# Performance work log

Hardware: AMD Instinct MI355X
Metric: run time of the kernel (lower is better)

Reference implementation:

```python
import jax, jax.numpy as jnp
import numpy as np

B, T, C, H = 4, 4096, 1024, 64

def setup_inputs() -> dict:
    key = jax.random.key(0)
    kx, kk, kq, kv = jax.random.split(key, 4)
    x = jax.random.normal(kx, (B, T, C), dtype=jnp.float32)
    # causal lower-triangular mask; masked_fill where mask == 0
    mask = jnp.tril(jnp.ones((T, T), dtype=jnp.int32))
    s = 1.0 / np.sqrt(C)
    Wk = jax.random.normal(kk, (H, C), dtype=jnp.float32) * s
    Wq = jax.random.normal(kq, (H, C), dtype=jnp.float32) * s
    Wv = jax.random.normal(kv, (H, C), dtype=jnp.float32) * s
    return {"x": x, "mask": mask, "Wk": Wk, "Wq": Wq, "Wv": Wv}

def reference(x, mask, Wk, Wq, Wv):
    # single-head attention; dropout is identity in eval mode
    scale = Wk.shape[0] ** -0.5  # head_size ** -0.5
    k = jnp.einsum('btc,hc->bth', x, Wk)  # [B,T,H]
    q = jnp.einsum('btc,hc->bth', x, Wq)
    v = jnp.einsum('btc,hc->bth', x, Wv)
    att = jnp.einsum('bqh,bkh->bqk', q, k) * scale  # [B,T,T]
    att = jnp.where(mask == 0, -jnp.inf, att)
    att = jax.nn.softmax(att, axis=-1)
    out = jnp.einsum('bqk,bkh->bqh', att, v)  # [B,T,H]
    return out
```

## Files before the change

kernel.cpp:

```cpp
#include <hip/hip_runtime.h>
#include <hip/hip_bf16.h>

#define BT 16384
#define CDIM 1024
#define HD 64
#define TT 4096

typedef __bf16 bf16x8 __attribute__((ext_vector_type(8)));
typedef __bf16 bf16x4 __attribute__((ext_vector_type(4)));
typedef float f32x4 __attribute__((ext_vector_type(4)));

__device__ __forceinline__ f32x4 mfma16(bf16x8 a, bf16x8 b, f32x4 c){
  return __builtin_amdgcn_mfma_f32_16x16x32_bf16(a, b, c, 0, 0, 0);
}

__global__ __launch_bounds__(256) void wconv_k(const float* __restrict__ Wk,
    const float* __restrict__ Wq, const float* __restrict__ Wv,
    __bf16* __restrict__ Wbf){
  int idx = blockIdx.x*256 + threadIdx.x;
  int e0 = idx*4;
  int n = e0 >> 10;
  int c = e0 & 1023;
  const float* src; float s;
  if (n < 64)      { src = Wk + (size_t)n*CDIM;       s = 1.0f;   }
  else if (n < 128){ src = Wq + (size_t)(n-64)*CDIM;  s = 0.125f; }
  else             { src = Wv + (size_t)(n-128)*CDIM; s = 1.0f;   }
  float4 v = *reinterpret_cast<const float4*>(src + c);
  __bf16* dst = Wbf + e0;
  dst[0]=(__bf16)(v.x*s); dst[1]=(__bf16)(v.y*s);
  dst[2]=(__bf16)(v.z*s); dst[3]=(__bf16)(v.w*s);
}

__global__ __launch_bounds__(256) void proj_k(const float* __restrict__ x,
    const __bf16* __restrict__ Wbf, __bf16* __restrict__ kb,
    __bf16* __restrict__ qb, __bf16* __restrict__ vTb){
  __shared__ __bf16 Wt[192][68];
  __shared__ __bf16 Xt[16][68];

  const int tid  = threadIdx.x;
  const int lane = tid & 63;
  const int w    = tid >> 6;
  const int l15  = lane & 15, g = lane >> 4;
  const long row0 = (long)blockIdx.x*16;

  int wrw[6], wc8[6];
  #pragma unroll
  for (int i=0;i<6;i++){
    const int c = tid + 256*i;
    wrw[i] = c >> 3;
    wc8[i] = (c & 7)*8;
  }
  const int xrw = tid >> 4, xc4 = (tid & 15)*4;
  const float* xsrc = x + (row0 + xrw)*CDIM + xc4;

  f32x4 acc[3];
  #pragma unroll
  for (int j=0;j<3;j++) acc[j] = (f32x4)(0.0f);

  bf16x8 wreg[6];
  float4 xr;

  #pragma unroll
  for (int i=0;i<6;i++)
    wreg[i] = *reinterpret_cast<const bf16x8*>(Wbf + (size_t)wrw[i]*CDIM + wc8[i]);
  xr = *reinterpret_cast<const float4*>(xsrc);

  for (int t=0; t<16; ++t){
    #pragma unroll
    for (int i=0;i<6;i++)
      *reinterpret_cast<bf16x8*>(&Wt[wrw[i]][wc8[i]]) = wreg[i];
    {
      bf16x4 xv;
      xv[0]=(__bf16)xr.x; xv[1]=(__bf16)xr.y; xv[2]=(__bf16)xr.z; xv[3]=(__bf16)xr.w;
      *reinterpret_cast<bf16x4*>(&Xt[xrw][xc4]) = xv;
    }
    __syncthreads();

    if (t+1 < 16){
      const int nk = (t+1)*64;
      #pragma unroll
      for (int i=0;i<6;i++)
        wreg[i] = *reinterpret_cast<const bf16x8*>(Wbf + (size_t)wrw[i]*CDIM + nk + wc8[i]);
      xr = *reinterpret_cast<const float4*>(xsrc + nk);
    }

    {
      bf16x8 a0 = *reinterpret_cast<const bf16x8*>(&Xt[l15][g*8]);
      bf16x8 a1 = *reinterpret_cast<const bf16x8*>(&Xt[l15][g*8 + 32]);
      #pragma unroll
      for (int nf=0;nf<3;nf++){
        bf16x8 b0 = *reinterpret_cast<const bf16x8*>(&Wt[w*48 + nf*16 + l15][g*8]);
        bf16x8 b1 = *reinterpret_cast<const bf16x8*>(&Wt[w*48 + nf*16 + l15][g*8 + 32]);
        acc[nf] = mfma16(a1, b1, mfma16(a0, b0, acc[nf]));
      }
    }
    __syncthreads();
  }

  const long bidx = row0 >> 12;
  #pragma unroll
  for (int nf=0;nf<3;nf++){
    const int n0  = w*48 + nf*16 + l15;
    const int mat = n0 >> 6;
    const int h   = n0 & 63;
    const long rbase = row0 + g*4;
    if (mat == 0){
      #pragma unroll
      for (int r=0;r<4;r++) kb[(rbase+r)*HD + h] = (__bf16)acc[nf][r];
    } else if (mat == 1){
      #pragma unroll
      for (int r=0;r<4;r++) qb[(rbase+r)*HD + h] = (__bf16)acc[nf][r];
    } else {
      bf16x4 t4;
      #pragma unroll
      for (int r=0;r<4;r++) t4[r] = (__bf16)acc[nf][r];
      *reinterpret_cast<bf16x4*>(vTb + (bidx*64 + h)*TT + (rbase & 4095)) = t4;
    }
  }
}

template<int NS>
__global__ __launch_bounds__(256) void attn_part_k(const __bf16* __restrict__ kbg,
    const __bf16* __restrict__ qbg, const __bf16* __restrict__ vT,
    __bf16* __restrict__ po, float* __restrict__ pl){
  __shared__ __bf16 Klds[64][68];
  __shared__ __bf16 Vlds[64][68];
  __shared__ __bf16 Plds[4][16][68];

  const int tid  = threadIdx.x;
  const int lane = tid & 63;
  const int w    = tid >> 6;
  const int l15  = lane & 15, g = lane >> 4;

  const int bi  = blockIdx.x;
  const int b   = bi / (64*NS);
  const int rem = bi % (64*NS);
  const int qt  = 63 - rem / NS;
  const int s   = rem % NS;

  const int ntiles = qt + 1;
  const int lo = ( s      * ntiles) / NS;
  const int hi = ((s + 1) * ntiles) / NS;
  const int pidx = (b*64 + qt)*NS + s;

  if (lo == hi){
    if (l15 == 0){
      #pragma unroll
      for (int r=0;r<4;r++) pl[pidx*64 + w*16 + g*4 + r] = 0.0f;
    }
    return;
  }

  const long qbase = (long)b*TT + (long)qt*64;

  bf16x8 qf0, qf1;
  {
    const __bf16* src = qbg + (qbase + w*16 + l15)*HD + g*8;
    qf0 = *reinterpret_cast<const bf16x8*>(src);
    qf1 = *reinterpret_cast<const bf16x8*>(src + 32);
  }

  f32x4 o[4];
  #pragma unroll
  for (int ch=0; ch<4; ++ch) o[ch] = (f32x4)(0.0f);
  float lp[4] = {0.f, 0.f, 0.f, 0.f};

  const __bf16* vbase = vT + (size_t)b*64*TT;

  const int skey = tid >> 2;
  const int sd0  = (tid & 3) * 16;
  bf16x8 kr0, kr1, vr0, vr1;

  {
    const long kvbase = (long)b*TT + (long)lo*64;
    const __bf16* ks = kbg + (kvbase + skey)*HD + sd0;
    kr0 = *reinterpret_cast<const bf16x8*>(ks);
    kr1 = *reinterpret_cast<const bf16x8*>(ks+8);
    const __bf16* vs = vbase + (size_t)skey*TT + lo*64 + sd0;
    vr0 = *reinterpret_cast<const bf16x8*>(vs);
    vr1 = *reinterpret_cast<const bf16x8*>(vs+8);
  }

  for (int kv=lo; kv<hi; ++kv){
    __syncthreads();
    *reinterpret_cast<bf16x8*>(&Klds[skey][sd0])   = kr0;
    *reinterpret_cast<bf16x8*>(&Klds[skey][sd0+8]) = kr1;
    *reinterpret_cast<bf16x8*>(&Vlds[skey][sd0])   = vr0;
    *reinterpret_cast<bf16x8*>(&Vlds[skey][sd0+8]) = vr1;
    __syncthreads();

    if (kv+1 < hi){
      const long nbase = (long)b*TT + (long)(kv+1)*64;
      const __bf16* ks = kbg + (nbase + skey)*HD + sd0;
      kr0 = *reinterpret_cast<const bf16x8*>(ks);
      kr1 = *reinterpret_cast<const bf16x8*>(ks+8);
      const __bf16* vs = vbase + (size_t)skey*TT + (kv+1)*64 + sd0;
      vr0 = *reinterpret_cast<const bf16x8*>(vs);
      vr1 = *reinterpret_cast<const bf16x8*>(vs+8);
    }

    f32x4 sv[4];
    __builtin_amdgcn_s_setprio(1);
    #pragma unroll
    for (int c=0;c<4;c++){
      bf16x8 kb0 = *reinterpret_cast<const bf16x8*>(&Klds[c*16 + l15][g*8]);
      bf16x8 kb1 = *reinterpret_cast<const bf16x8*>(&Klds[c*16 + l15][g*8 + 32]);
      sv[c] = mfma16(qf0, kb0, (f32x4)(-16.0f));
      sv[c] = mfma16(qf1, kb1, sv[c]);
    }
    __builtin_amdgcn_s_setprio(0);

    if (kv == qt){
      #pragma unroll
      for (int c=0;c<4;c++){
        const int key = c*16 + l15;
        #pragma unroll
        for (int r=0;r<4;r++){
          const int qr = w*16 + g*4 + r;
          if (key > qr) sv[c][r] = -1e30f;
        }
      }
    }

    #pragma unroll
    for (int c=0;c<4;c++){
      #pragma unroll
      for (int r=0;r<4;r++) sv[c][r] = __expf(sv[c][r]);
    }
    #pragma unroll
    for (int r=0;r<4;r++)
      lp[r] += (sv[0][r] + sv[1][r]) + (sv[2][r] + sv[3][r]);

    #pragma unroll
    for (int c=0;c<4;c++){
      #pragma unroll
      for (int r=0;r<4;r++) Plds[w][g*4+r][c*16 + l15] = (__bf16)sv[c][r];
    }
    asm volatile("s_waitcnt lgkmcnt(0)" ::: "memory");
    __builtin_amdgcn_sched_barrier(0);
    bf16x8 pa0 = *reinterpret_cast<const bf16x8*>(&Plds[w][l15][g*8]);
    bf16x8 pa1 = *reinterpret_cast<const bf16x8*>(&Plds[w][l15][g*8 + 32]);

    __builtin_amdgcn_s_setprio(1);
    #pragma unroll
    for (int ch=0; ch<4; ++ch){
      bf16x8 vb0 = *reinterpret_cast<const bf16x8*>(&Vlds[ch*16 + l15][g*8]);
      bf16x8 vb1 = *reinterpret_cast<const bf16x8*>(&Vlds[ch*16 + l15][g*8 + 32]);
      o[ch] = mfma16(pa0, vb0, o[ch]);
      o[ch] = mfma16(pa1, vb1, o[ch]);
    }
    __builtin_amdgcn_s_setprio(0);
  }

  float lr[4];
  #pragma unroll
  for (int r=0;r<4;r++){
    float v = lp[r];
    v += __shfl_xor(v, 1);
    v += __shfl_xor(v, 2);
    v += __shfl_xor(v, 4);
    v += __shfl_xor(v, 8);
    lr[r] = v;
  }
  float rl[4];
  #pragma unroll
  for (int r=0;r<4;r++) rl[r] = (lr[r] > 0.0f) ? 1.0f/lr[r] : 0.0f;

  __bf16* podst = po + (size_t)pidx*4096;
  #pragma unroll
  for (int ch=0; ch<4; ++ch){
    #pragma unroll
    for (int r=0;r<4;r++)
      podst[(w*16 + g*4 + r)*64 + ch*16 + l15] = (__bf16)(o[ch][r] * rl[r]);
  }
  if (l15 == 0){
    #pragma unroll
    for (int r=0;r<4;r++) pl[pidx*64 + w*16 + g*4 + r] = lr[r];
  }
}

template<int NS>
__global__ __launch_bounds__(256) void comb_k(const __bf16* __restrict__ po,
    const float* __restrict__ pl, float* __restrict__ out){
  const int idx4  = (blockIdx.x*256 + threadIdx.x)*4;
  const int qrow  = idx4 >> 6;
  const int dim0  = idx4 & 63;
  const int qtg   = qrow >> 6;
  const int rowin = qrow & 63;

  float num0=0.f, num1=0.f, num2=0.f, num3=0.f, den=0.f;
  #pragma unroll
  for (int s=0;s<NS;s++){
    const float lv = pl[(qtg*NS + s)*64 + rowin];
    den += lv;
    bf16x4 p4 = *reinterpret_cast<const bf16x4*>(
        po + (size_t)(qtg*NS + s)*4096 + rowin*64 + dim0);
    num0 += lv*(float)p4[0]; num1 += lv*(float)p4[1];
    num2 += lv*(float)p4[2]; num3 += lv*(float)p4[3];
  }
  const float rd = 1.0f/den;
  float4 o = make_float4(num0*rd, num1*rd, num2*rd, num3*rd);
  *reinterpret_cast<float4*>(out + idx4) = o;
}

extern "C" void kernel_launch(void* const* d_in, const int* in_sizes, int n_in,
                              void* d_out, int out_size, void* d_ws, size_t ws_size,
                              hipStream_t stream) {
  const float* x  = (const float*)d_in[0];
  const float* Wk = (const float*)d_in[2];
  const float* Wq = (const float*)d_in[3];
  const float* Wv = (const float*)d_in[4];
  float* out = (float*)d_out;

  char* ws = (char*)d_ws;
  __bf16* Wbf = (__bf16*)ws;
  __bf16* kb  = (__bf16*)(ws + 393216);
  __bf16* qb  = (__bf16*)(ws + 2490368);
  __bf16* vTb = (__bf16*)(ws + 4587520);
  __bf16* po  = (__bf16*)(ws + 6684672);

  wconv_k<<<192,  256, 0, stream>>>(Wk, Wq, Wv, Wbf);
  proj_k <<<1024, 256, 0, stream>>>(x, Wbf, kb, qb, vTb);

  const size_t need8 = 6684672ull + (size_t)2048*4096*2 + (size_t)2048*64*4;
  if (ws_size >= need8){
    float* pl = (float*)(ws + 6684672 + (size_t)2048*4096*2);
    attn_part_k<8><<<2048, 256, 0, stream>>>(kb, qb, vTb, po, pl);
    comb_k<8>    <<<1024, 256, 0, stream>>>(po, pl, out);
  } else {
    float* pl = (float*)(ws + 6684672 + (size_t)1024*4096*2);
    attn_part_k<4><<<1024, 256, 0, stream>>>(kb, qb, vTb, po, pl);
    comb_k<4>    <<<1024, 256, 0, stream>>>(po, pl, out);
  }
}
```

Measured before the change: 66.92 us.

## Enlarge projection tile to 32 rows and 128-wide K steps with 8 waves

The QKV projection kernel now processes 32 rows per block with 512 threads, split into two row-groups of four waves, and steps K by 128 instead of 64. Each staged weight tile is therefore reused across twice as many rows, which halves total weight traffic from global memory and halves the number of barrier iterations. The cost is larger LDS use per block (about 60 KB), possibly lower occupancy, and half as many blocks in the grid.

```diff
diff --git a/kernel.cpp b/kernel.cpp
--- a/kernel.cpp
+++ b/kernel.cpp
@@ -31,79 +31,97 @@
   dst[2]=(__bf16)(v.z*s); dst[3]=(__bf16)(v.w*s);
 }
 
-__global__ __launch_bounds__(256) void proj_k(const float* __restrict__ x,
+__global__ __launch_bounds__(512) void proj_k(const float* __restrict__ x,
     const __bf16* __restrict__ Wbf, __bf16* __restrict__ kb,
     __bf16* __restrict__ qb, __bf16* __restrict__ vTb){
-  __shared__ __bf16 Wt[192][68];
-  __shared__ __bf16 Xt[16][68];
+  __shared__ __bf16 Wt[192][136];
+  __shared__ __bf16 Xt[32][136];
 
   const int tid  = threadIdx.x;
   const int lane = tid & 63;
   const int w    = tid >> 6;
+  const int wr   = w >> 2;
+  const int wn   = w & 3;
   const int l15  = lane & 15, g = lane >> 4;
-  const long row0 = (long)blockIdx.x*16;
-
-  int wrw[6], wc8[6];
+  const long row0 = (long)blockIdx.x*32;
+
+  int wrw[6], wc16[6];
   #pragma unroll
   for (int i=0;i<6;i++){
-    const int c = tid + 256*i;
-    wrw[i] = c >> 3;
-    wc8[i] = (c & 7)*8;
-  }
-  const int xrw = tid >> 4, xc4 = (tid & 15)*4;
-  const float* xsrc = x + (row0 + xrw)*CDIM + xc4;
+    const int c = tid + 512*i;
+    wrw[i]  = c >> 4;
+    wc16[i] = (c & 15)*8;
+  }
+  int xrw[2], xc4[2];
+  #pragma unroll
+  for (int j=0;j<2;j++){
+    const int i2 = tid + 512*j;
+    xrw[j] = i2 >> 5;
+    xc4[j] = (i2 & 31)*4;
+  }
 
   f32x4 acc[3];
   #pragma unroll
   for (int j=0;j<3;j++) acc[j] = (f32x4)(0.0f);
 
   bf16x8 wreg[6];
-  float4 xr;
+  float4 xreg[2];
 
   #pragma unroll
   for (int i=0;i<6;i++)
-    wreg[i] = *reinterpret_cast<const bf16x8*>(Wbf + (size_t)wrw[i]*CDIM + wc8[i]);
-  xr = *reinterpret_cast<const float4*>(xsrc);
-
-  for (int t=0; t<16; ++t){
+    wreg[i] = *reinterpret_cast<const bf16x8*>(Wbf + (size_t)wrw[i]*CDIM + wc16[i]);
+  #pragma unroll
+  for (int j=0;j<2;j++)
+    xreg[j] = *reinterpret_cast<const float4*>(x + (row0 + xrw[j])*CDIM + xc4[j]);
+
+  for (int t=0; t<8; ++t){
     #pragma unroll
     for (int i=0;i<6;i++)
-      *reinterpret_cast<bf16x8*>(&Wt[wrw[i]][wc8[i]]) = wreg[i];
+      *reinterpret_cast<bf16x8*>(&Wt[wrw[i]][wc16[i]]) = wreg[i];
+    #pragma unroll
+    for (int j=0;j<2;j++){
+      bf16x4 xv;
+      xv[0]=(__bf16)xreg[j].x; xv[1]=(__bf16)xreg[j].y;
+      xv[2]=(__bf16)xreg[j].z; xv[3]=(__bf16)xreg[j].w;
+      *reinterpret_cast<bf16x4*>(&Xt[xrw[j]][xc4[j]]) = xv;
+    }
+    __syncthreads();
+
+    if (t+1 < 8){
+      const int nk = (t+1)*128;
+      #pragma unroll
+      for (int i=0;i<6;i++)
+        wreg[i] = *reinterpret_cast<const bf16x8*>(
+            Wbf + (size_t)wrw[i]*CDIM + nk + wc16[i]);
+      #pragma unroll
+      for (int j=0;j<2;j++)
+        xreg[j] = *reinterpret_cast<const float4*>(
+            x + (row0 + xrw[j])*CDIM + nk + xc4[j]);
+    }
+
     {
-      bf16x4 xv;
-      xv[0]=(__bf16)xr.x; xv[1]=(__bf16)xr.y; xv[2]=(__bf16)xr.z; xv[3]=(__bf16)xr.w;
-      *reinterpret_cast<bf16x4*>(&Xt[xrw][xc4]) = xv;
+      const __bf16* arow = &Xt[wr*16 + l15][0];
+      #pragma unroll
+      for (int kk=0; kk<4; ++kk){
+        bf16x8 a = *reinterpret_cast<const bf16x8*>(arow + kk*32 + g*8);
+        #pragma unroll
+        for (int nf=0;nf<3;nf++){
+          bf16x8 b = *reinterpret_cast<const bf16x8*>(
+              &Wt[wn*48 + nf*16 + l15][kk*32 + g*8]);
+          acc[nf] = mfma16(a, b, acc[nf]);
+        }
+      }
     }
     __syncthreads();
-
-    if (t+1 < 16){
-      const int nk = (t+1)*64;
-      #pragma unroll
-      for (int i=0;i<6;i++)
-        wreg[i] = *reinterpret_cast<const bf16x8*>(Wbf + (size_t)wrw[i]*CDIM + nk + wc8[i]);
-      xr = *reinterpret_cast<const float4*>(xsrc + nk);
-    }
-
-    {
-      bf16x8 a0 = *reinterpret_cast<const bf16x8*>(&Xt[l15][g*8]);
-      bf16x8 a1 = *reinterpret_cast<const bf16x8*>(&Xt[l15][g*8 + 32]);
-      #pragma unroll
-      for (int nf=0;nf<3;nf++){
-        bf16x8 b0 = *reinterpret_cast<const bf16x8*>(&Wt[w*48 + nf*16 + l15][g*8]);
-        bf16x8 b1 = *reinterpret_cast<const bf16x8*>(&Wt[w*48 + nf*16 + l15][g*8 + 32]);
-        acc[nf] = mfma16(a1, b1, mfma16(a0, b0, acc[nf]));
-      }
-    }
-    __syncthreads();
   }
 
   const long bidx = row0 >> 12;
   #pragma unroll
   for (int nf=0;nf<3;nf++){
-    const int n0  = w*48 + nf*16 + l15;
+    const int n0  = wn*48 + nf*16 + l15;
     const int mat = n0 >> 6;
     const int h   = n0 & 63;
-    const long rbase = row0 + g*4;
+    const long rbase = row0 + wr*16 + g*4;
     if (mat == 0){
       #pragma unroll
       for (int r=0;r<4;r++) kb[(rbase+r)*HD + h] = (__bf16)acc[nf][r];
@@ -319,8 +337,8 @@
   __bf16* vTb = (__bf16*)(ws + 4587520);
   __bf16* po  = (__bf16*)(ws + 6684672);
 
-  wconv_k<<<192,  256, 0, stream>>>(Wk, Wq, Wv, Wbf);
-  proj_k <<<1024, 256, 0, stream>>>(x, Wbf, kb, qb, vTb);
+  wconv_k<<<192, 256, 0, stream>>>(Wk, Wq, Wv, Wbf);
+  proj_k <<<512, 512, 0, stream>>>(x, Wbf, kb, qb, vTb);
 
   const size_t need8 = 6684672ull + (size_t)2048*4096*2 + (size_t)2048*64*4;
   if (ws_size >= need8){
```

Result: faster. 61.91 us (-7.5%).
